# Performance work log

Hardware: AMD Instinct MI355X
Metric: run time of the kernel (lower is better)

## Reference

```python
import jax, jax.numpy as jnp
import numpy as np

L_KERNELS = 15
STRIDE = 1
DIMS = [60, 72, 86, 86, 71, 59]  # indim=4*15, then *1.2,*1.2, mid, /1.2,/1.2 per __init__


def setup_inputs() -> dict:
    key = jax.random.key(0)
    ks = jax.random.split(key, 13)
    B, C, L, K = 16, 4, 1000, 64
    inp = {"x": jax.random.normal(ks[0], (B, C, L), jnp.float32)}
    for i in range(5):
        di, do = DIMS[i], DIMS[i + 1]
        inp[f"w{i}"] = jax.random.normal(ks[1 + 2 * i], (K, di, do), jnp.float32) * (1.0 / np.sqrt(di))
        inp[f"b{i}"] = jax.random.normal(ks[2 + 2 * i], (K, do), jnp.float32) * 0.01
    inp["head_w"] = jax.random.normal(ks[11], (DIMS[5], 1), jnp.float32) * (1.0 / np.sqrt(DIMS[5]))
    inp["head_b"] = jax.random.normal(ks[12], (1,), jnp.float32) * 0.01
    return inp


def reference(x, w0, b0, w1, b1, w2, b2, w3, b3, w4, b4, head_w, head_b):
    B, C, L = x.shape
    l, s = L_KERNELS, STRIDE
    n_out = (L - l) // s + 1
    # unfold: (B, C, n_out, l) via gather of sliding windows
    idx = jnp.arange(n_out)[:, None] * s + jnp.arange(l)[None, :]
    xw = x[:, :, idx]
    # transpose(-2,-3) then flatten(start_dim=3): (B, n_out, C*l)
    xw = jnp.transpose(xw, (0, 2, 1, 3)).reshape(B, n_out, C * l)
    # per-kernel FC stack: broadcast-mul+sum in torch == grouped matmul here
    h = jax.nn.gelu(jnp.einsum('bld,kde->bkle', xw, w0) + b0[None, :, None, :], approximate=False)
    for w, b in ((w1, b1), (w2, b2), (w3, b3), (w4, b4)):
        h = jax.nn.gelu(jnp.einsum('bkld,kde->bkle', h, w) + b[None, :, None, :], approximate=False)
    out = (h @ head_w + head_b).squeeze(-1)  # (B, K, n_out)
    return out
```

## Files before the change

### kernel.cpp

```cpp
#include <hip/hip_runtime.h>

typedef _Float16 f16;
typedef __attribute__((ext_vector_type(8))) _Float16 f16x8;
typedef __attribute__((ext_vector_type(2))) __fp16 hf16x2;
typedef __attribute__((ext_vector_type(4))) float f32x4;

constexpr int C_ = 4, L_ = 1000, K_ = 64, NOUT = 986, NPOS = 16 * 986;
constexpr int TPB  = 256;
constexpr int MTB  = 128;
constexpr int NBLK = (NPOS + MTB - 1) / MTB;
constexpr int AST  = 104;
constexpr int ACT_EL  = MTB * AST;
constexpr size_t SMEM_BYTES = (size_t)ACT_EL * 2 + 480 * 4 + 64 * 4;

constexpr size_t WOFF[5]  = {0, 638976, 1277952, 1916928, 2555904};
constexpr int    WROWS[5] = {80, 96, 96, 80, 64};
constexpr int    DIv[5]   = {60, 72, 86, 86, 71};
constexpr int    DOv[5]   = {72, 86, 86, 71, 59};
constexpr size_t WTOT    = WOFF[4] + (size_t)K_ * 96 * AST;
constexpr size_t ACT_WS  = WTOT;
constexpr size_t WS_NEED = (WTOT + (size_t)NBLK * ACT_EL) * 2;

constexpr int WUNITS = 5 * K_ * 2;
constexpr int AUNITS = NBLK * 2;

__device__ __forceinline__ float gelu_f(float x) {
    float s = x * x;
    float h = __builtin_fmaf(s, 5.1706e-8f, -2.86589e-6f);
    h = __builtin_fmaf(s, h, 6.96071e-5f);
    h = __builtin_fmaf(s, h, -9.95530e-4f);
    h = __builtin_fmaf(s, h, 9.54057e-3f);
    h = __builtin_fmaf(s, h, -6.60672e-2f);
    h = __builtin_fmaf(s, h, 3.988475e-1f);
    float q = __builtin_fmaf(x, h, 0.5f);
    q = fminf(fmaxf(q, 0.f), 1.f);
    return x * q;
}

template<int MT>
__device__ __forceinline__ void pre_a(const f16* __restrict__ wsrc, f16x8 (&ap)[6],
                                      int li, int q) {
#pragma unroll
    for (int mt = 0; mt < MT; mt++)
        ap[mt] = *(const f16x8*)(wsrc + (mt * 16 + li) * AST + q * 8);
}

template<int KSTEPS, int MT>
__device__ __forceinline__ void layer_mm_p(const f16* __restrict__ actw,
                                           const f16* __restrict__ wsrc,
                                           const f16x8 (&ap)[6],
                                           f32x4 (&acc)[MT][2],
                                           const float* __restrict__ bl, int li, int q) {
#pragma unroll
    for (int mt = 0; mt < MT; mt++) {
        f32x4 bb = *(const f32x4*)(bl + mt * 16 + q * 4);
#pragma unroll
        for (int nt = 0; nt < 2; nt++) acc[mt][nt] = bb;
    }
#pragma unroll
    for (int ks = 0; ks < KSTEPS; ks++) {
        const int koff = ks * 32 + q * 8;
        f16x8 a[MT], b[2];
#pragma unroll
        for (int mt = 0; mt < MT; mt++)
            a[mt] = (ks == 0) ? ap[mt]
                              : *(const f16x8*)(wsrc + (mt * 16 + li) * AST + koff);
#pragma unroll
        for (int nt = 0; nt < 2; nt++)
            b[nt] = *(const f16x8*)(actw + (nt * 16 + li) * AST + koff);
#pragma unroll
        for (int mt = 0; mt < MT; mt++)
#pragma unroll
            for (int nt = 0; nt < 2; nt++)
                acc[mt][nt] = __builtin_amdgcn_mfma_f32_16x16x32_f16(a[mt], b[nt], acc[mt][nt], 0, 0, 0);
    }
}

template<int MT>
__device__ __forceinline__ void epilogue(f32x4 (&acc)[MT][2], f16* __restrict__ actw,
                                         int li, int q) {
#pragma unroll
    for (int mt = 0; mt < MT; mt++) {
        const int eb = mt * 16 + q * 4;
#pragma unroll
        for (int nt = 0; nt < 2; nt++) {
            union { hf16x2 h[2]; unsigned long long u; } pk;
            pk.h[0] = __builtin_amdgcn_cvt_pkrtz(gelu_f(acc[mt][nt][0]),
                                                 gelu_f(acc[mt][nt][1]));
            pk.h[1] = __builtin_amdgcn_cvt_pkrtz(gelu_f(acc[mt][nt][2]),
                                                 gelu_f(acc[mt][nt][3]));
            f16* dst = actw + (nt * 16 + li) * AST + eb;
            *(unsigned long long*)dst = pk.u;
        }
    }
}

template<int L>
__device__ __forceinline__ void prep_one_half(const float* __restrict__ wsrc0,
                                              f16* __restrict__ ws, f16* __restrict__ wl,
                                              int k, int h, int tid) {
    constexpr int DI = DIv[L], DO = DOv[L], RW = WROWS[L];
    const float* wsrc = wsrc0 + (size_t)k * DI * DO;
    constexpr int TOT = DI * DO;
    constexpr int NIT = (TOT + 255) / 256;
    float v[NIT];
#pragma unroll
    for (int it = 0; it < NIT; it++) {
        int i = tid + it * 256;
        v[it] = (i < TOT) ? wsrc[i] : 0.f;
    }
#pragma unroll
    for (int it = 0; it < NIT; it++) {
        int i = tid + it * 256;
        if (i < TOT) {
            int d = i / DO, e = i - d * DO;
            wl[d * 87 + e] = (f16)v[it];
        }
    }
    __syncthreads();
    f16* dst = ws + WOFF[L] + (size_t)k * 96 * AST;
    constexpr int HCH = (RW / 2) * 13;
    constexpr int NIT2 = (HCH + 255) / 256;
#pragma unroll
    for (int it = 0; it < NIT2; it++) {
        int c0 = tid + it * 256;
        if (c0 < HCH) {
            int c = h * HCH + c0;
            int e = c / 13, db = (c - e * 13) * 8;
            f16x8 vv;
#pragma unroll
            for (int j = 0; j < 8; j++) {
                int d = db + j;
                vv[j] = (e < DO && d < DI) ? wl[d * 87 + e] : (f16)0.f;
            }
            *(f16x8*)(dst + (size_t)c * 8) = vv;
        }
    }
}

__device__ __forceinline__ void prep_act_half(const float* __restrict__ x,
                                              f16* __restrict__ dst0, int m, int h, int tid) {
    if (m >= NBLK) return;
    f16* dst = dst0 + (size_t)m * ACT_EL;
    const int base = m * MTB;
    constexpr int HCHK = MTB * 13 / 2;
    for (int i0 = tid; i0 < HCHK; i0 += 256) {
        int i = h * HCHK + i0;
        int r = i / 13, cc = (i - r * 13) * 8;
        int p = base + r; if (p > NPOS - 1) p = NPOS - 1;
        int b = p / NOUT, pos = p - b * NOUT;
        f16x8 vv;
#pragma unroll
        for (int j = 0; j < 8; j++) {
            int c = cc + j;
            float v = 0.f;
            if (c < 60) { int ch = c / 15, jj = c - ch * 15; v = x[(size_t)(b * C_ + ch) * L_ + pos + jj]; }
            vv[j] = (f16)v;
        }
        *(f16x8*)(dst + (size_t)r * AST + cc) = vv;
    }
}

__global__ __launch_bounds__(256) void prep_all(
    const float* __restrict__ w0, const float* __restrict__ w1, const float* __restrict__ w2,
    const float* __restrict__ w3, const float* __restrict__ w4,
    const float* __restrict__ x, f16* __restrict__ ws) {
    __shared__ f16 wl[86 * 87];
    const int tid = threadIdx.x, u = blockIdx.x;
    if (u < WUNITS) {
        const int k = (u >> 1) & 63, h = u & 1;
        switch (u >> 7) {
            case 0: prep_one_half<0>(w0, ws, wl, k, h, tid); break;
            case 1: prep_one_half<1>(w1, ws, wl, k, h, tid); break;
            case 2: prep_one_half<2>(w2, ws, wl, k, h, tid); break;
            case 3: prep_one_half<3>(w3, ws, wl, k, h, tid); break;
            default: prep_one_half<4>(w4, ws, wl, k, h, tid); break;
        }
    } else {
        const int v = u - WUNITS;
        prep_act_half(x, ws + ACT_WS, v >> 1, v & 1, tid);
    }
}

template<bool PRE>
__global__ __launch_bounds__(TPB, 5) void mlp_main(
    const float* __restrict__ x,
    const float* __restrict__ b0, const float* __restrict__ b1, const float* __restrict__ b2,
    const float* __restrict__ b3, const float* __restrict__ b4,
    const float* __restrict__ hw, const float* __restrict__ hb,
    const f16* __restrict__ ws, float* __restrict__ out) {
    extern __shared__ char smemraw[];
    f16*   act   = (f16*)smemraw;
    float* biasl = (float*)(act + ACT_EL);
    float* headl = biasl + 480;

    const int tid = threadIdx.x, k = blockIdx.x, mblk = blockIdx.y;
    const int wv = tid >> 6, lane = tid & 63, li = lane & 15, q = lane >> 4;
    const int base = mblk * MTB;
    f16* actw = act + (wv * 32) * AST;
    const f16* wk = ws + (size_t)k * 96 * AST;

    f16x8 ap[6];
    pre_a<5>(wk + WOFF[0], ap, li, q);

    for (int i = tid; i < 480; i += TPB) {
        int l = i / 96, e = i - l * 96;
        const float* bg = (l == 0) ? b0 : (l == 1) ? b1 : (l == 2) ? b2 : (l == 3) ? b3 : b4;
        int DO = (l == 0) ? 72 : (l == 1) ? 86 : (l == 2) ? 86 : (l == 3) ? 71 : 59;
        biasl[i] = (e < DO) ? bg[k * DO + e] : 0.f;
    }
    if (tid < 64) headl[tid] = (tid < 59) ? hw[tid] : 0.f;

    if constexpr (PRE) {
        const f16* src = ws + ACT_WS + (size_t)mblk * ACT_EL;
        for (int c = wv; c < 26; c += 4) {
            __builtin_amdgcn_global_load_lds(
                (const __attribute__((address_space(1))) void*)(src + c * 512 + lane * 8),
                (__attribute__((address_space(3))) void*)(act + c * 512), 16, 0, 0);
        }
    } else {
        const int b0i = base / NOUT;
        const int thr = (b0i + 1) * NOUT;
        for (int i = tid; i < 64 * MTB; i += TPB) {
            int d = i >> 7, r = i & (MTB - 1);
            int p = base + r; if (p > NPOS - 1) p = NPOS - 1;
            int b = (p >= thr) ? b0i + 1 : b0i;
            int pos = p - b * NOUT;
            float v = 0.f;
            if (d < 60) { int c = d / 15, j = d - c * 15; v = x[(size_t)(b * C_ + c) * L_ + pos + j]; }
            act[r * AST + d] = (f16)v;
        }
        for (int i = tid; i < MTB * 2; i += TPB) {
            int r = i >> 1, cc = (i & 1) << 3;
            *(f16x8*)(act + r * AST + 80 + cc) = f16x8{0,0,0,0,0,0,0,0};
        }
    }
    const float hb0 = hb[0];
    __syncthreads();

    f32x4 acc[6][2];
    f32x4 (&acc5)[5][2] = reinterpret_cast<f32x4 (&)[5][2]>(acc);

    layer_mm_p<2, 5>(actw, wk + WOFF[0], ap, acc5, biasl + 0 * 96, li, q);
    pre_a<6>(wk + WOFF[1], ap, li, q);
    epilogue<5>(acc5, actw, li, q);
    layer_mm_p<3, 6>(actw, wk + WOFF[1], ap, acc, biasl + 1 * 96, li, q);
    pre_a<6>(wk + WOFF[2], ap, li, q);
    epilogue<6>(acc, actw, li, q);
    layer_mm_p<3, 6>(actw, wk + WOFF[2], ap, acc, biasl + 2 * 96, li, q);
    pre_a<5>(wk + WOFF[3], ap, li, q);
    epilogue<6>(acc, actw, li, q);
    layer_mm_p<3, 5>(actw, wk + WOFF[3], ap, acc5, biasl + 3 * 96, li, q);
    pre_a<4>(wk + WOFF[4], ap, li, q);
    epilogue<5>(acc5, actw, li, q);

    f32x4 acc4[4][2];
    layer_mm_p<3, 4>(actw, wk + WOFF[4], ap, acc4, biasl + 4 * 96, li, q);
    float sum[2] = {0.f, 0.f};
#pragma unroll
    for (int mt = 0; mt < 4; mt++) {
        const int eb = mt * 16 + q * 4;
        f32x4 hh = *(const f32x4*)(headl + eb);
#pragma unroll
        for (int nt = 0; nt < 2; nt++) {
#pragma unroll
            for (int r = 0; r < 4; r++)
                sum[nt] += gelu_f(acc4[mt][nt][r]) * hh[r];
        }
    }
#pragma unroll
    for (int nt = 0; nt < 2; nt++) {
        float s = sum[nt];
        s += __shfl_xor(s, 16);
        s += __shfl_xor(s, 32);
        s += hb0;
        if (lane < 16) {
            int p = base + wv * 32 + nt * 16 + lane;
            if (p < NPOS) {
                int b = p / NOUT, pos = p - b * NOUT;
                out[((size_t)(b * K_ + k)) * NOUT + pos] = s;
            }
        }
    }
}

extern "C" void kernel_launch(void* const* d_in, const int* in_sizes, int n_in,
                              void* d_out, int out_size, void* d_ws, size_t ws_size,
                              hipStream_t stream) {
    const float* x  = (const float*)d_in[0];
    const float* w0 = (const float*)d_in[1];  const float* b0 = (const float*)d_in[2];
    const float* w1 = (const float*)d_in[3];  const float* b1 = (const float*)d_in[4];
    const float* w2 = (const float*)d_in[5];  const float* b2 = (const float*)d_in[6];
    const float* w3 = (const float*)d_in[7];  const float* b3 = (const float*)d_in[8];
    const float* w4 = (const float*)d_in[9];  const float* b4 = (const float*)d_in[10];
    const float* hw = (const float*)d_in[11]; const float* hb = (const float*)d_in[12];
    float* out = (float*)d_out;
    f16* ws = (f16*)d_ws;

    const bool pre = (ws_size >= WS_NEED);

    if (pre) {
        (void)hipFuncSetAttribute((const void*)mlp_main<true>,
                                  hipFuncAttributeMaxDynamicSharedMemorySize, (int)SMEM_BYTES);
        prep_all<<<dim3(WUNITS + AUNITS), 256, 0, stream>>>(w0, w1, w2, w3, w4, x, ws);
        mlp_main<true><<<dim3(K_, NBLK), TPB, SMEM_BYTES, stream>>>(
            x, b0, b1, b2, b3, b4, hw, hb, ws, out);
    } else {
        (void)hipFuncSetAttribute((const void*)mlp_main<false>,
                                  hipFuncAttributeMaxDynamicSharedMemorySize, (int)SMEM_BYTES);
        prep_all<<<dim3(WUNITS), 256, 0, stream>>>(w0, w1, w2, w3, w4, x, ws);
        mlp_main<false><<<dim3(K_, NBLK), TPB, SMEM_BYTES, stream>>>(
            x, b0, b1, b2, b3, b4, hw, hb, ws, out);
    }
}
```

Baseline: 256.5 us.

## Interleave weight layout per lane and split GELU between exp and polynomial forms

Weights are stored in a lane-major layout (row e placed at (e&15)*624 + (e>>4)*104), so each lane's MFMA A-operand rows sit contiguously behind one base pointer instead of being computed per tile. The GELU epilogue now alternates tiles between a sigmoid-based approximation (exp2 plus reciprocal on the transcendental unit) and a cheaper polynomial with med3 clamping. The aim is to balance VALU and transcendental throughput in the epilogue and cut address arithmetic in the matmul loops. The sigmoid form is a looser approximation of exact GELU, which may affect accuracy.

```diff
diff --git a/kernel.cpp b/kernel.cpp
--- a/kernel.cpp
+++ b/kernel.cpp
@@ -13,6 +13,9 @@
 constexpr int ACT_EL  = MTB * AST;
 constexpr size_t SMEM_BYTES = (size_t)ACT_EL * 2 + 480 * 4 + 64 * 4;
 
+__device__ __host__ __forceinline__ constexpr int wofs(int e, int col) {
+    return (e & 15) * 624 + (e >> 4) * 104 + col;
+}
 constexpr size_t WOFF[5]  = {0, 638976, 1277952, 1916928, 2555904};
 constexpr int    WROWS[5] = {80, 96, 96, 80, 64};
 constexpr int    DIv[5]   = {60, 72, 86, 86, 71};
@@ -24,7 +27,13 @@
 constexpr int WUNITS = 5 * K_ * 2;
 constexpr int AUNITS = NBLK * 2;
 
-__device__ __forceinline__ float gelu_f(float x) {
+__device__ __forceinline__ float gelu_t(float x) {
+    float x2 = x * x;
+    float ei = x * __builtin_fmaf(-0.1029433270f, x2, -2.3022082020f);
+    float e  = __builtin_amdgcn_exp2f(ei);
+    return x * __builtin_amdgcn_rcpf(e + 1.0f);
+}
+__device__ __forceinline__ float gelu_p(float x) {
     float s = x * x;
     float h = __builtin_fmaf(s, 5.1706e-8f, -2.86589e-6f);
     h = __builtin_fmaf(s, h, 6.96071e-5f);
@@ -32,17 +41,17 @@
     h = __builtin_fmaf(s, h, 9.54057e-3f);
     h = __builtin_fmaf(s, h, -6.60672e-2f);
     h = __builtin_fmaf(s, h, 3.988475e-1f);
-    float q = __builtin_fmaf(x, h, 0.5f);
-    q = fminf(fmaxf(q, 0.f), 1.f);
-    return x * q;
+    float y = __builtin_fmaf(s, h, 0.5f * x);
+    return __builtin_amdgcn_fmed3f(y, 0.f, x);
 }
 
 template<int MT>
 __device__ __forceinline__ void pre_a(const f16* __restrict__ wsrc, f16x8 (&ap)[6],
                                       int li, int q) {
+    const f16* wli = wsrc + li * 624;
 #pragma unroll
     for (int mt = 0; mt < MT; mt++)
-        ap[mt] = *(const f16x8*)(wsrc + (mt * 16 + li) * AST + q * 8);
+        ap[mt] = *(const f16x8*)(wli + mt * 104 + q * 8);
 }
 
 template<int KSTEPS, int MT>
@@ -57,6 +66,7 @@
 #pragma unroll
         for (int nt = 0; nt < 2; nt++) acc[mt][nt] = bb;
     }
+    const f16* wli = wsrc + li * 624;
 #pragma unroll
     for (int ks = 0; ks < KSTEPS; ks++) {
         const int koff = ks * 32 + q * 8;
@@ -64,7 +74,7 @@
 #pragma unroll
         for (int mt = 0; mt < MT; mt++)
             a[mt] = (ks == 0) ? ap[mt]
-                              : *(const f16x8*)(wsrc + (mt * 16 + li) * AST + koff);
+                              : *(const f16x8*)(wli + mt * 104 + koff);
 #pragma unroll
         for (int nt = 0; nt < 2; nt++)
             b[nt] = *(const f16x8*)(actw + (nt * 16 + li) * AST + koff);
@@ -85,10 +95,17 @@
 #pragma unroll
         for (int nt = 0; nt < 2; nt++) {
             union { hf16x2 h[2]; unsigned long long u; } pk;
-            pk.h[0] = __builtin_amdgcn_cvt_pkrtz(gelu_f(acc[mt][nt][0]),
-                                                 gelu_f(acc[mt][nt][1]));
-            pk.h[1] = __builtin_amdgcn_cvt_pkrtz(gelu_f(acc[mt][nt][2]),
-                                                 gelu_f(acc[mt][nt][3]));
+            if ((mt + nt) & 1) {
+                pk.h[0] = __builtin_amdgcn_cvt_pkrtz(gelu_p(acc[mt][nt][0]),
+                                                     gelu_p(acc[mt][nt][1]));
+                pk.h[1] = __builtin_amdgcn_cvt_pkrtz(gelu_p(acc[mt][nt][2]),
+                                                     gelu_p(acc[mt][nt][3]));
+            } else {
+                pk.h[0] = __builtin_amdgcn_cvt_pkrtz(gelu_t(acc[mt][nt][0]),
+                                                     gelu_t(acc[mt][nt][1]));
+                pk.h[1] = __builtin_amdgcn_cvt_pkrtz(gelu_t(acc[mt][nt][2]),
+                                                     gelu_t(acc[mt][nt][3]));
+            }
             f16* dst = actw + (nt * 16 + li) * AST + eb;
             *(unsigned long long*)dst = pk.u;
         }
@@ -133,7 +150,7 @@
                 int d = db + j;
                 vv[j] = (e < DO && d < DI) ? wl[d * 87 + e] : (f16)0.f;
             }
-            *(f16x8*)(dst + (size_t)c * 8) = vv;
+            *(f16x8*)(dst + wofs(e, db)) = vv;
         }
     }
 }
@@ -264,8 +281,10 @@
 #pragma unroll
         for (int nt = 0; nt < 2; nt++) {
 #pragma unroll
-            for (int r = 0; r < 4; r++)
-                sum[nt] += gelu_f(acc4[mt][nt][r]) * hh[r];
+            for (int r = 0; r < 4; r++) {
+                float g = ((mt + nt) & 1) ? gelu_p(acc4[mt][nt][r]) : gelu_t(acc4[mt][nt][r]);
+                sum[nt] += g * hh[r];
+            }
         }
     }
 #pragma unroll
```

New measurement: 265.4 us. 3.5% more time.
